# Optimization experiments

Measured on AMD Instinct MI355X. Metric: run time of the kernel, lower is better.

The kernel has to match this reference:

```python
import jax, jax.numpy as jnp
import numpy as np

IN_CH, OUT_CH, HID, NHEAD = 4, 1, 256, 8
VDIM = HID // NHEAD
LOCALITIES = (2.0, 10.0, 10.0, 10.0, 10.0, 200.0)
N_BLOCKS = len(LOCALITIES) - 2
INPUT_RES, LATENT_RES, OUTPUT_RES = (64, 64), (32, 32), (64, 64)
BATCH = 8


def pairwise_dist(res1x, res1y, res2x, res2y):
    gx1 = jnp.linspace(0, 1, res1x + 1)[:-1]
    gy1 = jnp.linspace(0, 1, res1y + 1)[:-1]
    g1x, g1y = jnp.meshgrid(gx1, gy1, indexing='xy')
    grid1 = jnp.stack([g1x.flatten(), g1y.flatten()], axis=-1)
    gx2 = jnp.linspace(0, 1, res2x + 1)[:-1]
    gy2 = jnp.linspace(0, 1, res2y + 1)[:-1]
    g2x, g2y = jnp.meshgrid(gx2, gy2, indexing='xy')
    grid2 = jnp.stack([g2x.flatten(), g2y.flatten()], axis=-1)
    diff = grid1[:, None, :] - grid2[None, :, :]
    return (jnp.sum(diff ** 2, axis=-1) / 2.0).astype(jnp.float32)


def pos_att(m_dist, x, r, w, locality):
    # m_dist:[Nq,Nk]  x:[B,Nk,HID]  r:[H,1,1]  w:[H,HID,VDIM]
    scale = jnp.tan(0.25 * jnp.pi * (1 - 1e-07) * (1 + jnp.sin(r)))
    sd = m_dist[None, :, :] * scale  # [H,Nq,Nk]
    if locality <= 100:
        thr = jnp.percentile(sd, locality, axis=-1, keepdims=True)
        sd = jnp.where(sd <= thr, sd, jnp.inf)
    att = jax.nn.softmax(-sd, axis=-1)  # [H,Nq,Nk]
    value = jnp.einsum('bnj,hjk->bhnk', x, w)  # [B,H,Nk,VDIM]
    out = jnp.einsum('hjn,bhnk->bhjk', att, value)  # [B,H,Nq,VDIM]
    out = jnp.transpose(out, (0, 2, 1, 3)).reshape(x.shape[0], m_dist.shape[0], -1)
    return jax.nn.gelu(out)


def lin(x, w, b):
    # eqx.nn.Linear: w:[out,in], b:[out]
    return jnp.einsum('bni,oi->bno', x, w) + b


def setup_inputs() -> dict:
    key = jax.random.key(0)
    ks = jax.random.split(key, 20)
    Ni = INPUT_RES[0] * INPUT_RES[1]
    s_h = 1.0 / jnp.sqrt(HID)
    s_in = 1.0 / jnp.sqrt(IN_CH)
    return {
        'x': jax.random.normal(ks[0], (BATCH, Ni, IN_CH), jnp.float32),
        'en_fc1_w': jax.random.uniform(ks[1], (HID, IN_CH), jnp.float32, -s_in, s_in),
        'en_fc1_b': jax.random.uniform(ks[2], (HID,), jnp.float32, -s_in, s_in),
        'down_r': jax.random.normal(ks[3], (NHEAD, 1, 1), jnp.float32),
        'down_w': jax.random.normal(ks[4], (NHEAD, HID, VDIM), jnp.float32) * s_h,
        'pa_r': jax.random.normal(ks[5], (N_BLOCKS, NHEAD, 1, 1), jnp.float32),
        'pa_w': jax.random.normal(ks[6], (N_BLOCKS, NHEAD, HID, VDIM), jnp.float32) * s_h,
        'mlp1_w': jax.random.uniform(ks[7], (N_BLOCKS, HID, HID), jnp.float32, -s_h, s_h),
        'mlp1_b': jax.random.uniform(ks[8], (N_BLOCKS, HID), jnp.float32, -s_h, s_h),
        'mlp2_w': jax.random.uniform(ks[9], (N_BLOCKS, HID, HID), jnp.float32, -s_h, s_h),
        'mlp2_b': jax.random.uniform(ks[10], (N_BLOCKS, HID), jnp.float32, -s_h, s_h),
        'res_w': jax.random.uniform(ks[11], (N_BLOCKS, HID, HID), jnp.float32, -s_h, s_h),
        'res_b': jax.random.uniform(ks[12], (N_BLOCKS, HID), jnp.float32, -s_h, s_h),
        'up_r': jax.random.normal(ks[13], (NHEAD, 1, 1), jnp.float32),
        'up_w': jax.random.normal(ks[14], (NHEAD, HID, VDIM), jnp.float32) * s_h,
        'de_fc1_w': jax.random.uniform(ks[15], (HID, HID), jnp.float32, -s_h, s_h),
        'de_fc1_b': jax.random.uniform(ks[16], (HID,), jnp.float32, -s_h, s_h),
        'de_fc2_w': jax.random.uniform(ks[17], (OUT_CH, HID), jnp.float32, -s_h, s_h),
        'de_fc2_b': jax.random.uniform(ks[18], (OUT_CH,), jnp.float32, -s_h, s_h),
    }


def reference(x, en_fc1_w, en_fc1_b, down_r, down_w, pa_r, pa_w,
              mlp1_w, mlp1_b, mlp2_w, mlp2_b, res_w, res_b,
              up_r, up_w, de_fc1_w, de_fc1_b, de_fc2_w, de_fc2_b):
    m_dist_down = pairwise_dist(LATENT_RES[0], LATENT_RES[1], INPUT_RES[0], INPUT_RES[1])
    m_dist_proc = pairwise_dist(LATENT_RES[0], LATENT_RES[1], LATENT_RES[0], LATENT_RES[1])
    m_dist_up = pairwise_dist(OUTPUT_RES[0], OUTPUT_RES[1], LATENT_RES[0], LATENT_RES[1])

    h = jax.nn.gelu(lin(x, en_fc1_w, en_fc1_b))
    h = pos_att(m_dist_down, h, down_r, down_w, LOCALITIES[0])
    for i in range(N_BLOCKS):
        pa_out = pos_att(m_dist_proc, h, pa_r[i], pa_w[i], LOCALITIES[1 + i])
        mlp_out = lin(jax.nn.gelu(lin(pa_out, mlp1_w[i], mlp1_b[i])), mlp2_w[i], mlp2_b[i])
        residual = lin(h, res_w[i], res_b[i])
        h = jax.nn.gelu(mlp_out + residual)
    h = pos_att(m_dist_up, h, up_r, up_w, LOCALITIES[-1])
    h = jax.nn.gelu(lin(h, de_fc1_w, de_fc1_b))
    return lin(h, de_fc2_w, de_fc2_b)
```

## Files before the change

kernel.cpp:

```cpp
#include <hip/hip_runtime.h>
#include <math.h>


#define PI_F 3.14159265358979323846f

typedef __attribute__((ext_vector_type(8))) short short8;
typedef __attribute__((ext_vector_type(4))) float float4v;
typedef __attribute__((ext_vector_type(4))) unsigned short ushort4v;

__device__ __forceinline__ float gelu_f(float x) {
  float u = 0.7978845608028654f * (x + 0.044715f * x * x * x);
  float e = __expf(2.0f * u);
  float t = 1.0f - 2.0f / (e + 1.0f);
  return 0.5f * x * (1.0f + t);
}

__device__ __forceinline__ float head_scale(float r) {
  return tanf(0.25f * PI_F * (1.0f - 1e-7f) * (1.0f + sinf(r)));
}

__device__ __forceinline__ unsigned short f2bf(float f) {
  union { float f; unsigned u; } c; c.f = f;
  unsigned u = c.u + 0x7FFFu + ((c.u >> 16) & 1u);
  return (unsigned short)(u >> 16);
}
__device__ __forceinline__ float bf2f(unsigned short h) {
  union { unsigned u; float f; } c; c.u = ((unsigned)h) << 16;
  return c.f;
}
__device__ __forceinline__ void split_bf(float f, unsigned short& hi,
                                         unsigned short& lo) {
  hi = f2bf(f);
  lo = f2bf(f - bf2f(hi));
}

__device__ __forceinline__ void gl16(const void* g, void* l) {
  __builtin_amdgcn_global_load_lds(
      (const __attribute__((address_space(1))) unsigned int*)g,
      (__attribute__((address_space(3))) unsigned int*)l, 16, 0, 0);
}

__global__ __launch_bounds__(256) void k_enc(
    const float* __restrict__ x, const float* __restrict__ w,
    const float* __restrict__ b, unsigned short* __restrict__ ahi,
    unsigned short* __restrict__ alo) {
  int row = blockIdx.x * 4 + (threadIdx.x >> 6);
  int o = (threadIdx.x & 63) * 4;
  float4 xv = *(const float4*)(x + (size_t)row * 4);
  ushort4v hv, lv;
#pragma unroll
  for (int i = 0; i < 4; ++i) {
    float4 wv = *(const float4*)(w + (size_t)(o + i) * 4);
    float s = xv.x * wv.x + xv.y * wv.y + xv.z * wv.z + xv.w * wv.w + b[o + i];
    s = gelu_f(s);
    unsigned short hi, lo;
    split_bf(s, hi, lo);
    hv[i] = hi; lv[i] = lo;
  }
  size_t idx = (size_t)row * 256 + o;
  *(ushort4v*)(ahi + idx) = hv;
  *(ushort4v*)(alo + idx) = lv;
}

__global__ __launch_bounds__(256) void k_split_all(
    const float* __restrict__ down_w, const float* __restrict__ de1_w,
    const float* __restrict__ up_w, const float* __restrict__ pa_w,
    const float* __restrict__ mlp1_w, const float* __restrict__ mlp2_w,
    const float* __restrict__ res_w, unsigned short* __restrict__ whi,
    unsigned short* __restrict__ wlo) {
  int i = blockIdx.x * 256 + threadIdx.x;
  float f;
  if (i < 65536) {
    int n = i >> 8, k = i & 255;
    f = down_w[(n >> 5) * 8192 + k * 32 + (n & 31)];
  } else if (i < 131072) {
    f = de1_w[i - 65536];
  } else if (i < 196608) {
    int j = i - 131072;
    int n = j >> 8, k = j & 255;
    f = up_w[(n >> 5) * 8192 + k * 32 + (n & 31)];
  } else if (i < 458752) {
    int j = i - 196608;
    int blk = j >> 16, r = j & 65535;
    int n = r >> 8, k = r & 255;
    f = pa_w[(size_t)blk * 65536 + (n >> 5) * 8192 + k * 32 + (n & 31)];
  } else if (i < 720896) {
    f = mlp1_w[i - 458752];
  } else if (i < 983040) {
    f = mlp2_w[i - 720896];
  } else {
    f = res_w[i - 983040];
  }
  unsigned short hi, lo;
  split_bf(f, hi, lo);
  whi[i] = hi;
  wlo[i] = lo;
}

template <int KRES, int CXM, int NPT, int TARGET, int TMAX>
__global__ __launch_bounds__(256) void k_thresh(int* __restrict__ thr) {
  __shared__ int wsum[4];
  int q = blockIdx.x, tid = threadIdx.x;
  int qx = q & 31, qy = q >> 5;
  int cx = qx * CXM, cy = qy * CXM;
  int d[NPT];
#pragma unroll
  for (int j = 0; j < NPT; ++j) {
    int k = tid * NPT + j;
    int kx = k & (KRES - 1), ky = k / KRES;
    int dx = cx - kx, dy = cy - ky;
    d[j] = dx * dx + dy * dy;
  }
  int lo = 0, hi = TMAX;
  while (lo < hi) {
    int mid = (lo + hi) >> 1;
    int c = 0;
#pragma unroll
    for (int j = 0; j < NPT; ++j) c += (d[j] <= mid) ? 1 : 0;
#pragma unroll
    for (int off = 32; off > 0; off >>= 1) c += __shfl_down(c, off, 64);
    if ((tid & 63) == 0) wsum[tid >> 6] = c;
    __syncthreads();
    int total = wsum[0] + wsum[1] + wsum[2] + wsum[3];
    __syncthreads();
    if (total >= TARGET) hi = mid; else lo = mid + 1;
  }
  if (tid == 0) thr[q] = lo;
}

template <int KRES, int CXM, int DSHIFT, int J2>
__global__ __launch_bounds__(256) void k_klist2(
    const float* __restrict__ rvec, const int* __restrict__ thr,
    int* __restrict__ klist2, int* __restrict__ kcnt2,
    float* __restrict__ wlist2) {
  __shared__ int cntS;
  __shared__ int sidx[J2];
  __shared__ int sdv[J2][4];
  __shared__ float denS[8][4];
  int tile = blockIdx.x, tid = threadIdx.x;
  int tx = tile & 15, ty = tile >> 4;
  int cxA[4], cyA[4], T[4];
#pragma unroll
  for (int i = 0; i < 4; ++i) {
    int qx = 2 * tx + (i & 1), qy = 2 * ty + (i >> 1);
    cxA[i] = qx * CXM; cyA[i] = qy * CXM;
    T[i] = thr[qy * 32 + qx];
  }
  if (tid == 0) cntS = 0;
  __syncthreads();
  int x0 = KRES - 1, x1 = 0, y0 = KRES - 1, y1 = 0;
#pragma unroll
  for (int i = 0; i < 4; ++i) {
    int rad = (int)sqrtf((float)T[i]);
    while ((rad + 1) * (rad + 1) <= T[i]) ++rad;
    while (rad > 0 && rad * rad > T[i]) --rad;
    x0 = min(x0, max(0, cxA[i] - rad));
    x1 = max(x1, min(KRES - 1, cxA[i] + rad));
    y0 = min(y0, max(0, cyA[i] - rad));
    y1 = max(y1, min(KRES - 1, cyA[i] + rad));
  }
  int W = x1 - x0 + 1, H = y1 - y0 + 1, tot = W * H;
  for (int p = tid; p < tot; p += 256) {
    int kx = x0 + p % W, ky = y0 + p / W;
    int d[4]; bool keep = false;
#pragma unroll
    for (int i = 0; i < 4; ++i) {
      int dx = cxA[i] - kx, dy = cyA[i] - ky;
      d[i] = dx * dx + dy * dy;
      keep = keep || (d[i] <= T[i]);
    }
    if (keep) {
      int s = atomicAdd(&cntS, 1);
      if (s < J2) {
        sidx[s] = ky * KRES + kx;
#pragma unroll
        for (int i = 0; i < 4; ++i) sdv[s][i] = d[i];
      }
    }
  }
  __syncthreads();
  int cnt = min(cntS, J2);
  int h = tid >> 5, lane = tid & 31;
  float sc = head_scale(rvec[h]) * (1.0f / (float)(1 << DSHIFT));
  float den[4] = {0.f, 0.f, 0.f, 0.f};
  for (int j = lane; j < cnt; j += 32) {
#pragma unroll
    for (int i = 0; i < 4; ++i)
      if (sdv[j][i] <= T[i]) den[i] += __expf(-sc * (float)sdv[j][i]);
  }
#pragma unroll
  for (int i = 0; i < 4; ++i) {
    float d0 = den[i];
#pragma unroll
    for (int off = 16; off > 0; off >>= 1) d0 += __shfl_down(d0, off, 32);
    if (lane == 0) denS[h][i] = d0;
  }
  __syncthreads();
  float inv[4];
#pragma unroll
  for (int i = 0; i < 4; ++i) inv[i] = 1.0f / denS[h][i];
  for (int j = lane; j < cnt; j += 32) {
    float w[4];
#pragma unroll
    for (int i = 0; i < 4; ++i)
      w[i] = (sdv[j][i] <= T[i]) ? __expf(-sc * (float)sdv[j][i]) * inv[i] : 0.f;
    float4v wv = {w[0], w[1], w[2], w[3]};
    *(float4v*)&wlist2[(((size_t)h * 256 + tile) * J2 + j) * 4] = wv;
  }
  if (tid == 0) kcnt2[tile] = cnt;
  if (h == 0)
    for (int j = lane; j < cnt; j += 32) klist2[(size_t)tile * J2 + j] = sidx[j];
}

template <int NK, int J2>
__global__ __launch_bounds__(256) void k_att3(
    const float* __restrict__ value,
    const int* __restrict__ klist2, const int* __restrict__ kcnt2,
    const float* __restrict__ wlist2, unsigned short* __restrict__ ohi,
    unsigned short* __restrict__ olo) {
  __shared__ int kls[J2];
  __shared__ float4v wls[J2];
  __shared__ float4v part[4][4][64];
  int blk = blockIdx.x;
  int tile = blk >> 3, h = blk & 7;
  int tid = threadIdx.x, g = tid & 63, s = tid >> 6;
  int cnt = kcnt2[tile];
  for (int j = tid; j < cnt; j += 256) {
    kls[j] = klist2[(size_t)tile * J2 + j];
    wls[j] = *(const float4v*)&wlist2[(((size_t)h * 256 + tile) * J2 + j) * 4];
  }
  __syncthreads();
  const float* vb = value + (size_t)h * NK * 256 + g * 4;
  float4v acc[4];
#pragma unroll
  for (int i = 0; i < 4; ++i) acc[i] = (float4v)0.0f;
  for (int j = s; j < cnt; j += 4) {
    int row = kls[j];
    float4v v = *(const float4v*)(vb + (size_t)row * 256);
    float4v w = wls[j];
    acc[0] += w.x * v;
    acc[1] += w.y * v;
    acc[2] += w.z * v;
    acc[3] += w.w * v;
  }
#pragma unroll
  for (int i = 0; i < 4; ++i) part[s][i][g] = acc[i];
  __syncthreads();
  if (tid < 64) {
    int g2 = tid;
    int ttx = tile & 15, tty = tile >> 4;
    int batch = g2 >> 3, v0 = (g2 & 7) * 4;
#pragma unroll
    for (int i = 0; i < 4; ++i) {
      float4v o4 = part[0][i][g2] + part[1][i][g2] + part[2][i][g2] +
                   part[3][i][g2];
      int q = (2 * tty + (i >> 1)) * 32 + 2 * ttx + (i & 1);
      size_t idx = ((size_t)batch * 1024 + q) * 256 + h * 32 + v0;
      ushort4v hv, lv;
#pragma unroll
      for (int c = 0; c < 4; ++c) {
        float oo = gelu_f(o4[c]);
        unsigned short hi, lo;
        split_bf(oo, hi, lo);
        hv[c] = hi; lv[c] = lo;
      }
      *(ushort4v*)(ohi + idx) = hv;
      *(ushort4v*)(olo + idx) = lv;
    }
  }
}

template <int BM, int BN, bool DUAL, int OL, bool GEL, bool OHILO>
__global__ __launch_bounds__(256) void k_gn(
    const unsigned short* __restrict__ A1hi, const unsigned short* __restrict__ A1lo,
    const unsigned short* __restrict__ W1hi, const unsigned short* __restrict__ W1lo,
    const unsigned short* __restrict__ A2hi, const unsigned short* __restrict__ A2lo,
    const unsigned short* __restrict__ W2hi, const unsigned short* __restrict__ W2lo,
    const float* __restrict__ bias, const float* __restrict__ bias2,
    float* __restrict__ outf, unsigned short* __restrict__ ohi,
    unsigned short* __restrict__ olo, int NS) {
  constexpr int MS = BM / 32;
  constexpr int NF = BN / 32;
  constexpr int NWCH = BN / 32;
  constexpr int NACH = BM / 32;
  __shared__ alignas(16) unsigned short Wh_s[2][BN * 64];
  __shared__ alignas(16) unsigned short Wl_s[2][BN * 64];
  __shared__ alignas(16) unsigned short Ah_s[2][BM * 64];
  __shared__ alignas(16) unsigned short Al_s[2][BM * 64];
  int tid = threadIdx.x;
  constexpr int BPM = 256 / BN;
  int b = blockIdx.x;
  int m0, n_off;
  if (BPM == 1) {
    m0 = b * BM; n_off = 0;
  } else {
    int x = b & 7, t = b >> 3;
    int nh = t & 1, mt = (t >> 1) * 8 + x;
    m0 = mt * BM; n_off = nh * BN;
  }
  int w = tid >> 6, lane = tid & 63;
  int quad = lane >> 4, l16 = lane & 15;
  int wm = (w >> 1) * (BM / 2), wn = (w & 1) * (BN / 2);

  int wgo[NWCH], wls_[NWCH];
#pragma unroll
  for (int i = 0; i < NWCH; ++i) {
    int rem = tid + i * 256;
    int r = rem >> 3, s = rem & 7, c = s ^ (r & 7);
    wgo[i] = (n_off + r) * 256 + c * 8;
    wls_[i] = rem * 8;
  }
  int ago[NACH], als_[NACH];
#pragma unroll
  for (int i = 0; i < NACH; ++i) {
    int rem = tid + i * 256;
    int r = rem >> 3, s = rem & 7, c = s ^ (r & 7);
    ago[i] = r * 256 + c * 8;
    als_[i] = rem * 8;
  }

  float4v acc[MS][NF];
#pragma unroll
  for (int i = 0; i < MS; ++i)
#pragma unroll
    for (int n = 0; n < NF; ++n) acc[i][n] = (float4v)0.0f;

  const int NSTEP = DUAL ? 8 : 4;

  auto STAGE = [&](int st, int buf) {
    const unsigned short *pWh, *pWl, *pAh, *pAl;
    if (DUAL && st >= 4) { pWh = W2hi; pWl = W2lo; pAh = A2hi; pAl = A2lo; }
    else { pWh = W1hi; pWl = W1lo; pAh = A1hi; pAl = A1lo; }
    int kb = (st & 3) * 64;
#pragma unroll
    for (int i = 0; i < NWCH; ++i) {
      gl16(pWh + wgo[i] + kb, &Wh_s[buf][wls_[i]]);
      gl16(pWl + wgo[i] + kb, &Wl_s[buf][wls_[i]]);
    }
    size_t ab = (size_t)m0 * 256 + kb;
#pragma unroll
    for (int i = 0; i < NACH; ++i) {
      gl16(pAh + ab + ago[i], &Ah_s[buf][als_[i]]);
      gl16(pAl + ab + ago[i], &Al_s[buf][als_[i]]);
    }
  };

  STAGE(0, 0);
  __syncthreads();
  for (int st = 0; st < NSTEP; ++st) {
    int cur = st & 1;
    if (st + 1 < NSTEP) STAGE(st + 1, cur ^ 1);
#pragma unroll
    for (int ks2 = 0; ks2 < 2; ++ks2) {
      short8 ah[MS], al[MS];
#pragma unroll
      for (int ms = 0; ms < MS; ++ms) {
        int ra = wm + ms * 16 + l16;
        int c = (ks2 * 4 + quad) ^ (ra & 7);
        ah[ms] = *(const short8*)&Ah_s[cur][ra * 64 + c * 8];
        al[ms] = *(const short8*)&Al_s[cur][ra * 64 + c * 8];
      }
#pragma unroll
      for (int ns = 0; ns < NF; ++ns) {
        int rb = wn + ns * 16 + l16;
        int c = (ks2 * 4 + quad) ^ (rb & 7);
        short8 bh = *(const short8*)&Wh_s[cur][rb * 64 + c * 8];
        short8 bl = *(const short8*)&Wl_s[cur][rb * 64 + c * 8];
#pragma unroll
        for (int ms = 0; ms < MS; ++ms) {
          acc[ms][ns] = __builtin_amdgcn_mfma_f32_16x16x32_bf16(
              ah[ms], bh, acc[ms][ns], 0, 0, 0);
          acc[ms][ns] = __builtin_amdgcn_mfma_f32_16x16x32_bf16(
              ah[ms], bl, acc[ms][ns], 0, 0, 0);
          acc[ms][ns] = __builtin_amdgcn_mfma_f32_16x16x32_bf16(
              al[ms], bh, acc[ms][ns], 0, 0, 0);
        }
      }
    }
    __syncthreads();
  }
#pragma unroll
  for (int ms = 0; ms < MS; ++ms) {
#pragma unroll
    for (int ns = 0; ns < NF; ++ns) {
      int n = n_off + wn + ns * 16 + l16;
      float bv = bias ? bias[n] : 0.0f;
      if (DUAL && bias2) bv += bias2[n];
#pragma unroll
      for (int r = 0; r < 4; ++r) {
        int m = m0 + wm + ms * 16 + quad * 4 + r;
        float c = acc[ms][ns][r] + bv;
        if (GEL) c = gelu_f(c);
        if (OHILO) {
          unsigned short chi, clo;
          split_bf(c, chi, clo);
          ohi[(size_t)m * 256 + n] = chi;
          olo[(size_t)m * 256 + n] = clo;
        } else if (OL == 0) {
          outf[(size_t)m * 256 + n] = c;
        } else {
          int N = 1 << NS;
          int bb = m >> NS, rr = m & (N - 1);
          outf[(((size_t)(n >> 5) * N + rr) * 8 + bb) * 32 + (n & 31)] = c;
        }
      }
    }
  }
}

__global__ __launch_bounds__(256) void k_up_s1(
    const float* __restrict__ value,
    const float* __restrict__ rvec, float* __restrict__ T) {
  __shared__ float AxL[64][33];
  int ky = blockIdx.x, h = blockIdx.y, tid = threadIdx.x;
  float sc = head_scale(rvec[h]) * (1.0f / 8192.0f);
  float v[32];
  const float* vb = value + ((size_t)h * 1024 + ky * 32) * 256 + tid;
#pragma unroll
  for (int kx = 0; kx < 32; ++kx) v[kx] = vb[kx * 256];
  if (tid < 64) {
    int qx = tid, dxmin = qx & 1;
    for (int kx = 0; kx < 32; ++kx) {
      int dx = qx - 2 * kx;
      AxL[qx][kx] = __expf(-sc * (float)(dx * dx - dxmin));
    }
  }
  __syncthreads();
  float* tb = T + (((size_t)h * 64) * 32 + ky) * 256 + tid;
  for (int qx = 0; qx < 64; ++qx) {
    float acc = 0.f;
#pragma unroll
    for (int kx = 0; kx < 32; ++kx) acc += AxL[qx][kx] * v[kx];
    tb[(size_t)qx * 32 * 256] = acc;
  }
}

__global__ __launch_bounds__(256) void k_up_s2(
    const float* __restrict__ T, const float* __restrict__ rvec,
    unsigned short* __restrict__ ohi, unsigned short* __restrict__ olo) {
  __shared__ float AyL[64][33];
  __shared__ float Sy[64];
  __shared__ float SxS;
  int qx = blockIdx.x, h = blockIdx.y, tid = threadIdx.x;
  float sc = head_scale(rvec[h]) * (1.0f / 8192.0f);
  float t[32];
  const float* tb = T + ((size_t)h * 64 + qx) * 32 * 256 + tid;
#pragma unroll
  for (int ky = 0; ky < 32; ++ky) t[ky] = tb[ky * 256];
  if (tid < 64) {
    int qy = tid, dymin = qy & 1;
    float s = 0.f;
    for (int ky = 0; ky < 32; ++ky) {
      int dy = qy - 2 * ky;
      float e = __expf(-sc * (float)(dy * dy - dymin));
      AyL[qy][ky] = e;
      s += e;
    }
    Sy[qy] = s;
  } else if (tid >= 64 && tid < 96) {
    int kx = tid - 64, dxmin = qx & 1;
    int dx = qx - 2 * kx;
    float e = __expf(-sc * (float)(dx * dx - dxmin));
#pragma unroll
    for (int off = 16; off > 0; off >>= 1) e += __shfl_down(e, off, 32);
    if (kx == 0) SxS = e;
  }
  __syncthreads();
  float invSx = 1.0f / SxS;
  int b = tid >> 5, v = tid & 31;
  size_t base = ((size_t)b * 4096 + qx) * 256 + h * 32 + v;
  for (int qy = 0; qy < 64; ++qy) {
    float acc = 0.f;
#pragma unroll
    for (int ky = 0; ky < 32; ++ky) acc += AyL[qy][ky] * t[ky];
    float o = gelu_f(acc * invSx / Sy[qy]);
    unsigned short hi, lo;
    split_bf(o, hi, lo);
    size_t idx = base + (size_t)qy * 64 * 256;
    ohi[idx] = hi;
    olo[idx] = lo;
  }
}

__global__ __launch_bounds__(256) void k_fc2(const float* __restrict__ h,
                                             const float* __restrict__ w,
                                             const float* __restrict__ b,
                                             float* __restrict__ out) {
  int row = blockIdx.x * 4 + (threadIdx.x >> 6);
  int lane = threadIdx.x & 63;
  float4 hv = *(const float4*)(h + (size_t)row * 256 + lane * 4);
  float4 wv = *(const float4*)(w + lane * 4);
  float s = hv.x * wv.x + hv.y * wv.y + hv.z * wv.z + hv.w * wv.w;
#pragma unroll
  for (int off = 32; off > 0; off >>= 1) s += __shfl_down(s, off, 64);
  if (lane == 0) out[row] = s + b[0];
}

extern "C" void kernel_launch(void* const* d_in, const int* in_sizes, int n_in,
                              void* d_out, int out_size, void* d_ws,
                              size_t ws_size, hipStream_t stream) {
  const float* x      = (const float*)d_in[0];
  const float* en_w   = (const float*)d_in[1];
  const float* en_b   = (const float*)d_in[2];
  const float* down_r = (const float*)d_in[3];
  const float* down_w = (const float*)d_in[4];
  const float* pa_r   = (const float*)d_in[5];
  const float* pa_w   = (const float*)d_in[6];
  const float* mlp1_w = (const float*)d_in[7];
  const float* mlp1_b = (const float*)d_in[8];
  const float* mlp2_w = (const float*)d_in[9];
  const float* mlp2_b = (const float*)d_in[10];
  const float* res_w  = (const float*)d_in[11];
  const float* res_b  = (const float*)d_in[12];
  const float* up_r   = (const float*)d_in[13];
  const float* up_w   = (const float*)d_in[14];
  const float* de1_w  = (const float*)d_in[15];
  const float* de1_b  = (const float*)d_in[16];
  const float* de2_w  = (const float*)d_in[17];
  const float* de2_b  = (const float*)d_in[18];
  float* out = (float*)d_out;

  constexpr int J2 = 256;
  float* ws = (float*)d_ws;
  unsigned short* Ahi = (unsigned short*)ws;
  unsigned short* Alo = Ahi + 8388608;
  float* B = ws + 8388608;
  float* Tbuf = B + 2097152;
  unsigned short* hAhi = (unsigned short*)(ws + 16777216);
  unsigned short* hAlo = hAhi + 2097152;
  unsigned short* hBhi = hAlo + 2097152;
  unsigned short* hBlo = hBhi + 2097152;
  unsigned short* pahi = hBlo + 2097152;
  unsigned short* palo = pahi + 2097152;
  unsigned short* m1hi = palo + 2097152;
  unsigned short* m1lo = m1hi + 2097152;
  int* thrD = (int*)(ws + 25165824);
  int* thrP = thrD + 1024;
  int* cntD2 = thrP + 1024;
  int* cntP2 = cntD2 + 256;
  int* klD2 = cntP2 + 256;
  int* klP2 = klD2 + 256 * J2;
  float* wlD2 = (float*)(klP2 + 256 * J2);
  float* wlP2 = wlD2 + 2097152;
  unsigned short* Whi = (unsigned short*)(wlP2 + 2097152);
  unsigned short* Wlo = Whi + 1245184;
  const int WO_DOWN = 0, WO_DE1 = 65536, WO_UP = 131072, WO_PA = 196608,
            WO_MLP1 = 458752, WO_MLP2 = 720896, WO_RES = 983040;

  k_enc<<<8192, 256, 0, stream>>>(x, en_w, en_b, Ahi, Alo);
  k_split_all<<<4864, 256, 0, stream>>>(down_w, de1_w, up_w, pa_w, mlp1_w,
                                        mlp2_w, res_w, Whi, Wlo);
  k_thresh<64, 2, 16, 82, 7938><<<1024, 256, 0, stream>>>(thrD);
  k_thresh<32, 1, 4, 103, 1922><<<1024, 256, 0, stream>>>(thrP);
  k_klist2<64, 2, 13, J2><<<256, 256, 0, stream>>>(down_r, thrD, klD2, cntD2,
                                                   wlD2);
  k_klist2<32, 1, 11, J2><<<256, 256, 0, stream>>>(pa_r, thrP, klP2, cntP2,
                                                   wlP2);
  k_gn<64, 256, false, 1, false, false><<<512, 256, 0, stream>>>(
      Ahi, Alo, Whi + WO_DOWN, Wlo + WO_DOWN, nullptr, nullptr, nullptr,
      nullptr, nullptr, nullptr, B, nullptr, nullptr, 12);
  k_att3<4096, J2><<<2048, 256, 0, stream>>>(B, klD2, cntD2, wlD2, hAhi, hAlo);
  for (int i = 0; i < 4; ++i) {
    const unsigned short* hih = (i & 1) ? hBhi : hAhi;
    const unsigned short* hil = (i & 1) ? hBlo : hAlo;
    unsigned short* hoh = (i & 1) ? hAhi : hBhi;
    unsigned short* hol = (i & 1) ? hAlo : hBlo;
    k_gn<32, 128, false, 1, false, false><<<512, 256, 0, stream>>>(
        hih, hil, Whi + WO_PA + i * 65536, Wlo + WO_PA + i * 65536, nullptr,
        nullptr, nullptr, nullptr, nullptr, nullptr, B, nullptr, nullptr, 10);
    k_att3<1024, J2><<<2048, 256, 0, stream>>>(B, klP2, cntP2, wlP2, pahi,
                                               palo);
    k_gn<32, 128, false, 0, true, true><<<512, 256, 0, stream>>>(
        pahi, palo, Whi + WO_MLP1 + i * 65536, Wlo + WO_MLP1 + i * 65536,
        nullptr, nullptr, nullptr, nullptr, mlp1_b + i * 256, nullptr, nullptr,
        m1hi, m1lo, 0);
    k_gn<32, 128, true, 0, true, true><<<512, 256, 0, stream>>>(
        m1hi, m1lo, Whi + WO_MLP2 + i * 65536, Wlo + WO_MLP2 + i * 65536, hih,
        hil, Whi + WO_RES + i * 65536, Wlo + WO_RES + i * 65536,
        mlp2_b + i * 256, res_b + i * 256, nullptr, hoh, hol, 0);
  }
  k_gn<32, 128, false, 1, false, false><<<512, 256, 0, stream>>>(
      hAhi, hAlo, Whi + WO_UP, Wlo + WO_UP, nullptr, nullptr, nullptr, nullptr,
      nullptr, nullptr, B, nullptr, nullptr, 10);
  k_up_s1<<<dim3(32, 8), 256, 0, stream>>>(B, up_r, Tbuf);
  k_up_s2<<<dim3(64, 8), 256, 0, stream>>>(Tbuf, up_r, Ahi, Alo);
  k_gn<64, 256, false, 0, true, false><<<512, 256, 0, stream>>>(
      Ahi, Alo, Whi + WO_DE1, Wlo + WO_DE1, nullptr, nullptr, nullptr, nullptr,
      de1_b, nullptr, B, nullptr, nullptr, 0);
  k_fc2<<<8192, 256, 0, stream>>>(B, de2_w, de2_b, out);
}
```

Measured before the change: 546.1 us.

## Stage full-K weight slice in LDS and stream activations from global memory

The GEMM kernel no longer double-buffers A and W tiles over K steps. It now loads the entire K=256 weight slice for a BN=64 column block into shared memory once, then reads activation fragments directly from global memory into registers. Tile shapes change to BM=64/128 with BN=64 and a 4-way N split across blocks, and the per-step synchronisation is removed. This trades LDS reuse of A, which is now fetched uncached per wave, for fewer barriers and larger weight reuse, and it raises the shared-memory footprint to 64 KB per block, which can limit occupancy.

Result: slower. 559.4 us (+2.4%).

```diff
diff --git a/kernel.cpp b/kernel.cpp
--- a/kernel.cpp
+++ b/kernel.cpp
@@ -271,7 +271,7 @@
 }
 
 template <int BM, int BN, bool DUAL, int OL, bool GEL, bool OHILO>
-__global__ __launch_bounds__(256) void k_gn(
+__global__ __launch_bounds__(256) void k_gw(
     const unsigned short* __restrict__ A1hi, const unsigned short* __restrict__ A1lo,
     const unsigned short* __restrict__ W1hi, const unsigned short* __restrict__ W1lo,
     const unsigned short* __restrict__ A2hi, const unsigned short* __restrict__ A2lo,
@@ -281,43 +281,26 @@
     unsigned short* __restrict__ olo, int NS) {
   constexpr int MS = BM / 32;
   constexpr int NF = BN / 32;
-  constexpr int NWCH = BN / 32;
-  constexpr int NACH = BM / 32;
-  __shared__ alignas(16) unsigned short Wh_s[2][BN * 64];
-  __shared__ alignas(16) unsigned short Wl_s[2][BN * 64];
-  __shared__ alignas(16) unsigned short Ah_s[2][BM * 64];
-  __shared__ alignas(16) unsigned short Al_s[2][BM * 64];
+  constexpr int NWR = BN / 8;
+  __shared__ alignas(16) unsigned short Wh_s[BN * 256];
+  __shared__ alignas(16) unsigned short Wl_s[BN * 256];
   int tid = threadIdx.x;
-  constexpr int BPM = 256 / BN;
   int b = blockIdx.x;
-  int m0, n_off;
-  if (BPM == 1) {
-    m0 = b * BM; n_off = 0;
-  } else {
-    int x = b & 7, t = b >> 3;
-    int nh = t & 1, mt = (t >> 1) * 8 + x;
-    m0 = mt * BM; n_off = nh * BN;
-  }
+  int x = b & 7, t = b >> 3;
+  int nq = t & 3, mt = (t >> 2) * 8 + x;
+  int m0 = mt * BM, n_off = nq * BN;
   int w = tid >> 6, lane = tid & 63;
   int quad = lane >> 4, l16 = lane & 15;
   int wm = (w >> 1) * (BM / 2), wn = (w & 1) * (BN / 2);
 
-  int wgo[NWCH], wls_[NWCH];
-#pragma unroll
-  for (int i = 0; i < NWCH; ++i) {
+  int wgo[NWR], wls_[NWR];
+#pragma unroll
+  for (int i = 0; i < NWR; ++i) {
     int rem = tid + i * 256;
-    int r = rem >> 3, s = rem & 7, c = s ^ (r & 7);
+    int r = rem >> 5, s = rem & 31, c = s ^ (r & 7);
     wgo[i] = (n_off + r) * 256 + c * 8;
     wls_[i] = rem * 8;
   }
-  int ago[NACH], als_[NACH];
-#pragma unroll
-  for (int i = 0; i < NACH; ++i) {
-    int rem = tid + i * 256;
-    int r = rem >> 3, s = rem & 7, c = s ^ (r & 7);
-    ago[i] = r * 256 + c * 8;
-    als_[i] = rem * 8;
-  }
 
   float4v acc[MS][NF];
 #pragma unroll
@@ -325,47 +308,36 @@
 #pragma unroll
     for (int n = 0; n < NF; ++n) acc[i][n] = (float4v)0.0f;
 
-  const int NSTEP = DUAL ? 8 : 4;
-
-  auto STAGE = [&](int st, int buf) {
-    const unsigned short *pWh, *pWl, *pAh, *pAl;
-    if (DUAL && st >= 4) { pWh = W2hi; pWl = W2lo; pAh = A2hi; pAl = A2lo; }
-    else { pWh = W1hi; pWl = W1lo; pAh = A1hi; pAl = A1lo; }
-    int kb = (st & 3) * 64;
-#pragma unroll
-    for (int i = 0; i < NWCH; ++i) {
-      gl16(pWh + wgo[i] + kb, &Wh_s[buf][wls_[i]]);
-      gl16(pWl + wgo[i] + kb, &Wl_s[buf][wls_[i]]);
-    }
-    size_t ab = (size_t)m0 * 256 + kb;
-#pragma unroll
-    for (int i = 0; i < NACH; ++i) {
-      gl16(pAh + ab + ago[i], &Ah_s[buf][als_[i]]);
-      gl16(pAl + ab + ago[i], &Al_s[buf][als_[i]]);
-    }
-  };
-
-  STAGE(0, 0);
-  __syncthreads();
-  for (int st = 0; st < NSTEP; ++st) {
-    int cur = st & 1;
-    if (st + 1 < NSTEP) STAGE(st + 1, cur ^ 1);
-#pragma unroll
-    for (int ks2 = 0; ks2 < 2; ++ks2) {
+  const int NPASS = DUAL ? 2 : 1;
+  for (int p = 0; p < NPASS; ++p) {
+    const unsigned short* pWh = p ? W2hi : W1hi;
+    const unsigned short* pWl = p ? W2lo : W1lo;
+    const unsigned short* pAh = p ? A2hi : A1hi;
+    const unsigned short* pAl = p ? A2lo : A1lo;
+    if (p) __syncthreads();
+#pragma unroll
+    for (int i = 0; i < NWR; ++i) {
+      gl16(pWh + wgo[i], &Wh_s[wls_[i]]);
+      gl16(pWl + wgo[i], &Wl_s[wls_[i]]);
+    }
+    __syncthreads();
+#pragma unroll
+    for (int ks2 = 0; ks2 < 8; ++ks2) {
       short8 ah[MS], al[MS];
 #pragma unroll
       for (int ms = 0; ms < MS; ++ms) {
-        int ra = wm + ms * 16 + l16;
-        int c = (ks2 * 4 + quad) ^ (ra & 7);
-        ah[ms] = *(const short8*)&Ah_s[cur][ra * 64 + c * 8];
-        al[ms] = *(const short8*)&Al_s[cur][ra * 64 + c * 8];
+        size_t off = (size_t)(m0 + wm + ms * 16 + l16) * 256 + ks2 * 32 +
+                     quad * 8;
+        ah[ms] = *(const short8*)(pAh + off);
+        al[ms] = *(const short8*)(pAl + off);
       }
 #pragma unroll
       for (int ns = 0; ns < NF; ++ns) {
-        int rb = wn + ns * 16 + l16;
-        int c = (ks2 * 4 + quad) ^ (rb & 7);
-        short8 bh = *(const short8*)&Wh_s[cur][rb * 64 + c * 8];
-        short8 bl = *(const short8*)&Wl_s[cur][rb * 64 + c * 8];
+        int lr = wn + ns * 16 + l16;
+        int L = ks2 * 4 + quad;
+        int so = lr * 256 + (L ^ (lr & 7)) * 8;
+        short8 bh = *(const short8*)&Wh_s[so];
+        short8 bl = *(const short8*)&Wl_s[so];
 #pragma unroll
         for (int ms = 0; ms < MS; ++ms) {
           acc[ms][ns] = __builtin_amdgcn_mfma_f32_16x16x32_bf16(
@@ -377,7 +349,6 @@
         }
       }
     }
-    __syncthreads();
   }
 #pragma unroll
   for (int ms = 0; ms < MS; ++ms) {
@@ -556,7 +527,7 @@
                                                    wlD2);
   k_klist2<32, 1, 11, J2><<<256, 256, 0, stream>>>(pa_r, thrP, klP2, cntP2,
                                                    wlP2);
-  k_gn<64, 256, false, 1, false, false><<<512, 256, 0, stream>>>(
+  k_gw<128, 64, false, 1, false, false><<<1024, 256, 0, stream>>>(
       Ahi, Alo, Whi + WO_DOWN, Wlo + WO_DOWN, nullptr, nullptr, nullptr,
       nullptr, nullptr, nullptr, B, nullptr, nullptr, 12);
   k_att3<4096, J2><<<2048, 256, 0, stream>>>(B, klD2, cntD2, wlD2, hAhi, hAlo);
@@ -565,26 +536,26 @@
     const unsigned short* hil = (i & 1) ? hBlo : hAlo;
     unsigned short* hoh = (i & 1) ? hAhi : hBhi;
     unsigned short* hol = (i & 1) ? hAlo : hBlo;
-    k_gn<32, 128, false, 1, false, false><<<512, 256, 0, stream>>>(
+    k_gw<64, 64, false, 1, false, false><<<512, 256, 0, stream>>>(
         hih, hil, Whi + WO_PA + i * 65536, Wlo + WO_PA + i * 65536, nullptr,
         nullptr, nullptr, nullptr, nullptr, nullptr, B, nullptr, nullptr, 10);
     k_att3<1024, J2><<<2048, 256, 0, stream>>>(B, klP2, cntP2, wlP2, pahi,
                                                palo);
-    k_gn<32, 128, false, 0, true, true><<<512, 256, 0, stream>>>(
+    k_gw<64, 64, false, 0, true, true><<<512, 256, 0, stream>>>(
         pahi, palo, Whi + WO_MLP1 + i * 65536, Wlo + WO_MLP1 + i * 65536,
         nullptr, nullptr, nullptr, nullptr, mlp1_b + i * 256, nullptr, nullptr,
         m1hi, m1lo, 0);
-    k_gn<32, 128, true, 0, true, true><<<512, 256, 0, stream>>>(
+    k_gw<64, 64, true, 0, true, true><<<512, 256, 0, stream>>>(
         m1hi, m1lo, Whi + WO_MLP2 + i * 65536, Wlo + WO_MLP2 + i * 65536, hih,
         hil, Whi + WO_RES + i * 65536, Wlo + WO_RES + i * 65536,
         mlp2_b + i * 256, res_b + i * 256, nullptr, hoh, hol, 0);
   }
-  k_gn<32, 128, false, 1, false, false><<<512, 256, 0, stream>>>(
+  k_gw<64, 64, false, 1, false, false><<<512, 256, 0, stream>>>(
       hAhi, hAlo, Whi + WO_UP, Wlo + WO_UP, nullptr, nullptr, nullptr, nullptr,
       nullptr, nullptr, B, nullptr, nullptr, 10);
   k_up_s1<<<dim3(32, 8), 256, 0, stream>>>(B, up_r, Tbuf);
   k_up_s2<<<dim3(64, 8), 256, 0, stream>>>(Tbuf, up_r, Ahi, Alo);
-  k_gn<64, 256, false, 0, true, false><<<512, 256, 0, stream>>>(
+  k_gw<128, 64, false, 0, true, false><<<1024, 256, 0, stream>>>(
       Ahi, Alo, Whi + WO_DE1, Wlo + WO_DE1, nullptr, nullptr, nullptr, nullptr,
       de1_b, nullptr, B, nullptr, nullptr, 0);
   k_fc2<<<8192, 256, 0, stream>>>(B, de2_w, de2_b, out);
```
